# Optimization experiments

Measured on AMD Instinct MI355X. Metric: run time of the kernel, lower is better.

Reference implementation:

```python
import jax, jax.numpy as jnp
import numpy as np

H = 2048          # hidden_size
N = 16384         # batch (= events processed in one forward)
THR = 0.7         # event_threshold
NEG = -1e30       # masked-softmax fill


def setup_inputs() -> dict:
    key = jax.random.key(0)
    ks = jax.random.split(key, 8)
    s = lambda k, shape, scale: (jax.random.normal(k, shape, dtype=jnp.float32) * scale)
    return {
        "x": jax.random.normal(ks[0], (N, H), dtype=jnp.float32),
        "importance": jax.random.uniform(ks[1], (N,), dtype=jnp.float32),
        # event_detector: Linear(H, H//2) -> ReLU -> Linear(H//2, 1) -> Sigmoid
        "W_e1": s(ks[2], (H, H // 2), 0.02), "b_e1": jnp.zeros((H // 2,), jnp.float32),
        "W_e2": s(ks[3], (H // 2, 1), 0.05), "b_e2": jnp.ones((1,), jnp.float32),
        # retrieval_network: Linear(H, H//2) -> ReLU -> Linear(H//2, H) -> Sigmoid
        "W_r1": s(ks[4], (H, H // 2), 0.02), "b_r1": jnp.zeros((H // 2,), jnp.float32),
        "W_r2": s(ks[5], (H // 2, H), 0.02), "b_r2": jnp.zeros((H,), jnp.float32),
        "timestamp": 0,
    }


def reference(x, importance, W_e1, b_e1, W_e2, b_e2, W_r1, b_r1, W_r2, b_r2, timestamp):
    # --- detect_events: MLP -> sigmoid -> threshold -------------------------
    scores = jax.nn.sigmoid(jnp.maximum(x @ W_e1 + b_e1, 0.0) @ W_e2 + b_e2)[:, 0]  # [N]
    events = scores > THR                                   # bool mask = event-gated scatter
    has_events = jnp.any(events)

    # --- store_memory + consolidate_memories --------------------------------
    # Event rows are written into the ring buffer (no wraparound since N <= capacity);
    # consolidation = softmax over stored importances, weighted sum of stored rows.
    logits = jnp.where(events, importance, NEG)             # masked softmax over event rows
    w = jax.nn.softmax(logits)                              # [N]
    w = jnp.where(events, w, 0.0)
    consolidated = w @ x                                    # [H]

    # --- retrieve_memory -----------------------------------------------------
    # After consolidation memory_count == 1, so softmax(similarities) == 1 for
    # every query row and retrieved_memory == consolidated (broadcast to [N,H]).
    retrieved = jax.nn.sigmoid(jnp.maximum(consolidated @ W_r1 + b_r1, 0.0) @ W_r2 + b_r2)  # [H]

    # If no events fired, memory_count == 0 and retrieve_memory returns zeros.
    add = jnp.where(has_events, retrieved, jnp.zeros_like(retrieved))
    return x + add[None, :]
```

## Files before the change

### kernel.cpp

```cpp
#include <hip/hip_runtime.h>
#include <hip/hip_bf16.h>

#define H_    2048
#define NROWS 16384
#define HH    1024

typedef __bf16 bf16x8 __attribute__((ext_vector_type(8)));
typedef float  floatx4 __attribute__((ext_vector_type(4)));

__device__ __forceinline__ unsigned f2bf(float f) {
  unsigned u = __builtin_bit_cast(unsigned, f);
  u += 0x7fff + ((u >> 16) & 1);
  return u >> 16;
}

__device__ __forceinline__ void gload_lds16(const void* g, void* l) {
  __builtin_amdgcn_global_load_lds(
      (const __attribute__((address_space(1))) unsigned*)g,
      (__attribute__((address_space(3))) unsigned*)l, 16, 0, 0);
}

__global__ __launch_bounds__(256) void convert_x_kernel(
    const float* __restrict__ x, unsigned short* __restrict__ xb)
{
  size_t i = ((size_t)blockIdx.x * 256 + threadIdx.x) * 8;
  float4 v0 = *reinterpret_cast<const float4*>(x + i);
  float4 v1 = *reinterpret_cast<const float4*>(x + i + 4);
  uint4 o;
  o.x = f2bf(v0.x) | (f2bf(v0.y) << 16);
  o.y = f2bf(v0.z) | (f2bf(v0.w) << 16);
  o.z = f2bf(v1.x) | (f2bf(v1.y) << 16);
  o.w = f2bf(v1.z) | (f2bf(v1.w) << 16);
  *reinterpret_cast<uint4*>(xb + i) = o;
}

__global__ __launch_bounds__(256) void transpose_w1_kernel(
    const float* __restrict__ W1, unsigned short* __restrict__ W1t)
{
  __shared__ unsigned short tile[64][66];
  int k0 = blockIdx.x * 64;
  int n0 = blockIdx.y * 64;
  int t = threadIdx.x;
#pragma unroll
  for (int i = 0; i < 4; i++) {
    int idx = t + i * 256;
    int r = idx >> 4, c4 = (idx & 15) << 2;
    float4 v = *reinterpret_cast<const float4*>(W1 + (size_t)(k0 + r) * HH + n0 + c4);
    tile[r][c4 + 0] = (unsigned short)f2bf(v.x);
    tile[r][c4 + 1] = (unsigned short)f2bf(v.y);
    tile[r][c4 + 2] = (unsigned short)f2bf(v.z);
    tile[r][c4 + 3] = (unsigned short)f2bf(v.w);
  }
  __syncthreads();
#pragma unroll
  for (int i = 0; i < 2; i++) {
    int idx = t + i * 256;
    int n = idx >> 3, k8 = (idx & 7) << 3;
    uint4 o;
    o.x = (unsigned)tile[k8 + 0][n] | ((unsigned)tile[k8 + 1][n] << 16);
    o.y = (unsigned)tile[k8 + 2][n] | ((unsigned)tile[k8 + 3][n] << 16);
    o.z = (unsigned)tile[k8 + 4][n] | ((unsigned)tile[k8 + 5][n] << 16);
    o.w = (unsigned)tile[k8 + 6][n] | ((unsigned)tile[k8 + 7][n] << 16);
    *reinterpret_cast<uint4*>(W1t + (size_t)(n0 + n) * H_ + k0 + k8) = o;
  }
}

__global__ __launch_bounds__(256) void gemm_v2_kernel(
    const unsigned short* __restrict__ xb, const unsigned short* __restrict__ W1t,
    const float* __restrict__ b1, const float* __restrict__ W2,
    float* __restrict__ s_pre)
{
  __shared__ unsigned short As[128 * 32];
  __shared__ unsigned short Bs[128 * 32];

  const int t    = threadIdx.x;
  const int n0   = blockIdx.x * 128;
  const int m0   = blockIdx.y * 128;
  const int wave = t >> 6, lane = t & 63;
  const int wr   = (wave >> 1) * 64;
  const int wc   = (wave & 1) * 64;
  const int lcol = lane & 15, quad = lane >> 4;

  floatx4 acc[4][4] = {};

  const unsigned short* ag0 = xb  + (size_t)(m0 + (t >> 2)) * H_ + (t & 3) * 8;
  const unsigned short* ag1 = ag0 + (size_t)64 * H_;
  const unsigned short* bg0 = W1t + (size_t)(n0 + (t >> 2)) * H_ + (t & 3) * 8;
  const unsigned short* bg1 = bg0 + (size_t)64 * H_;
  unsigned short* al0 = As + 512 * wave;
  unsigned short* al1 = As + 2048 + 512 * wave;
  unsigned short* bl0 = Bs + 512 * wave;
  unsigned short* bl1 = Bs + 2048 + 512 * wave;

  for (int kk = 0; kk < H_; kk += 32) {
    __syncthreads();
    gload_lds16(ag0 + kk, al0);
    gload_lds16(ag1 + kk, al1);
    gload_lds16(bg0 + kk, bl0);
    gload_lds16(bg1 + kk, bl1);
    __syncthreads();

    bf16x8 af[4], bfr[4];
#pragma unroll
    for (int mt = 0; mt < 4; mt++)
      af[mt] = *reinterpret_cast<const bf16x8*>(As + (wr + mt * 16 + lcol) * 32 + quad * 8);
#pragma unroll
    for (int nt = 0; nt < 4; nt++)
      bfr[nt] = *reinterpret_cast<const bf16x8*>(Bs + (wc + nt * 16 + lcol) * 32 + quad * 8);
#pragma unroll
    for (int mt = 0; mt < 4; mt++)
#pragma unroll
      for (int nt = 0; nt < 4; nt++)
        acc[mt][nt] = __builtin_amdgcn_mfma_f32_16x16x32_bf16(af[mt], bfr[nt], acc[mt][nt], 0, 0, 0);
  }

  float rowsum[4][4];
#pragma unroll
  for (int mt = 0; mt < 4; mt++)
#pragma unroll
    for (int r = 0; r < 4; r++) rowsum[mt][r] = 0.f;

#pragma unroll
  for (int nt = 0; nt < 4; nt++) {
    int n = n0 + wc + nt * 16 + lcol;
    float b1v = b1[n], w2v = W2[n];
#pragma unroll
    for (int mt = 0; mt < 4; mt++)
#pragma unroll
      for (int r = 0; r < 4; r++) {
        float h = fmaxf(acc[mt][nt][r] + b1v, 0.f);
        rowsum[mt][r] = fmaf(h, w2v, rowsum[mt][r]);
      }
  }
#pragma unroll
  for (int mt = 0; mt < 4; mt++)
#pragma unroll
    for (int r = 0; r < 4; r++) {
      float s = rowsum[mt][r];
      s += __shfl_xor(s, 1); s += __shfl_xor(s, 2);
      s += __shfl_xor(s, 4); s += __shfl_xor(s, 8);
      if (lcol == 0)
        atomicAdd(&s_pre[m0 + wr + mt * 16 + quad * 4 + r], s);
    }
}

__global__ __launch_bounds__(256) void gemm_score_kernel(
    const float* __restrict__ x, const float* __restrict__ W1,
    const float* __restrict__ b1, const float* __restrict__ W2,
    float* __restrict__ s_pre)
{
  __shared__ unsigned short As[128][40];
  __shared__ unsigned short Bs[128][40];
  const int t    = threadIdx.x;
  const int n0   = blockIdx.x * 128;
  const int m0   = blockIdx.y * 128;
  const int wave = t >> 6, lane = t & 63;
  const int wr   = (wave >> 1) * 64;
  const int wc   = (wave & 1) * 64;
  const int lcol = lane & 15, quad = lane >> 4;
  floatx4 acc[4][4] = {};

  for (int kk = 0; kk < H_; kk += 32) {
    __syncthreads();
#pragma unroll
    for (int i = 0; i < 4; i++) {
      int idx = t + i * 256;
      int row = idx >> 3, k4 = (idx & 7) << 2;
      float4 v = *reinterpret_cast<const float4*>(x + (size_t)(m0 + row) * H_ + kk + k4);
      unsigned lo = f2bf(v.x) | (f2bf(v.y) << 16);
      unsigned hi = f2bf(v.z) | (f2bf(v.w) << 16);
      *reinterpret_cast<uint2*>(&As[row][k4]) = make_uint2(lo, hi);
    }
#pragma unroll
    for (int i = 0; i < 4; i++) {
      int idx = t + i * 256;
      int kr = idx >> 5, c4 = (idx & 31) << 2;
      float4 v = *reinterpret_cast<const float4*>(W1 + (size_t)(kk + kr) * HH + n0 + c4);
      Bs[c4 + 0][kr] = (unsigned short)f2bf(v.x);
      Bs[c4 + 1][kr] = (unsigned short)f2bf(v.y);
      Bs[c4 + 2][kr] = (unsigned short)f2bf(v.z);
      Bs[c4 + 3][kr] = (unsigned short)f2bf(v.w);
    }
    __syncthreads();
    bf16x8 af[4], bfr[4];
#pragma unroll
    for (int mt = 0; mt < 4; mt++)
      af[mt] = *reinterpret_cast<const bf16x8*>(&As[wr + mt * 16 + lcol][quad * 8]);
#pragma unroll
    for (int nt = 0; nt < 4; nt++)
      bfr[nt] = *reinterpret_cast<const bf16x8*>(&Bs[wc + nt * 16 + lcol][quad * 8]);
#pragma unroll
    for (int mt = 0; mt < 4; mt++)
#pragma unroll
      for (int nt = 0; nt < 4; nt++)
        acc[mt][nt] = __builtin_amdgcn_mfma_f32_16x16x32_bf16(af[mt], bfr[nt], acc[mt][nt], 0, 0, 0);
  }
  float rowsum[4][4];
#pragma unroll
  for (int mt = 0; mt < 4; mt++)
#pragma unroll
    for (int r = 0; r < 4; r++) rowsum[mt][r] = 0.f;
#pragma unroll
  for (int nt = 0; nt < 4; nt++) {
    int n = n0 + wc + nt * 16 + lcol;
    float b1v = b1[n], w2v = W2[n];
#pragma unroll
    for (int mt = 0; mt < 4; mt++)
#pragma unroll
      for (int r = 0; r < 4; r++) {
        float h = fmaxf(acc[mt][nt][r] + b1v, 0.f);
        rowsum[mt][r] = fmaf(h, w2v, rowsum[mt][r]);
      }
  }
#pragma unroll
  for (int mt = 0; mt < 4; mt++)
#pragma unroll
    for (int r = 0; r < 4; r++) {
      float s = rowsum[mt][r];
      s += __shfl_xor(s, 1); s += __shfl_xor(s, 2);
      s += __shfl_xor(s, 4); s += __shfl_xor(s, 8);
      if (lcol == 0)
        atomicAdd(&s_pre[m0 + wr + mt * 16 + quad * 4 + r], s);
    }
}

__global__ __launch_bounds__(256) void score_kernel(
    const float* __restrict__ s_pre, const float* __restrict__ imp,
    const float* __restrict__ b2, float* __restrict__ wbuf,
    float* __restrict__ Z, float* __restrict__ cnt)
{
  int i = blockIdx.x * 256 + threadIdx.x;
  float s = s_pre[i] + b2[0];
  float sig = 1.f / (1.f + __expf(-s));
  bool ev = sig > 0.7f;
  float w = ev ? __expf(imp[i]) : 0.f;
  wbuf[i] = w;
  float cw = ev ? 1.f : 0.f;
#pragma unroll
  for (int off = 32; off; off >>= 1) {
    w  += __shfl_down(w, off);
    cw += __shfl_down(cw, off);
  }
  if ((threadIdx.x & 63) == 0) {
    atomicAdd(Z, w);
    atomicAdd(cnt, cw);
  }
}

__global__ __launch_bounds__(256) void consolidate_kernel(
    const float* __restrict__ x, const float* __restrict__ wbuf,
    float* __restrict__ c)
{
  int t = threadIdx.x;
  int r0 = blockIdx.x * 128;
  float a[8] = {0.f, 0.f, 0.f, 0.f, 0.f, 0.f, 0.f, 0.f};
  for (int r = 0; r < 128; r++) {
    float w = wbuf[r0 + r];
    if (w != 0.f) {
      const float4* xr = reinterpret_cast<const float4*>(x + (size_t)(r0 + r) * H_);
      float4 v0 = xr[t], v1 = xr[t + 256];
      a[0] = fmaf(w, v0.x, a[0]); a[1] = fmaf(w, v0.y, a[1]);
      a[2] = fmaf(w, v0.z, a[2]); a[3] = fmaf(w, v0.w, a[3]);
      a[4] = fmaf(w, v1.x, a[4]); a[5] = fmaf(w, v1.y, a[5]);
      a[6] = fmaf(w, v1.z, a[6]); a[7] = fmaf(w, v1.w, a[7]);
    }
  }
  int j0 = t * 4;
  atomicAdd(&c[j0 + 0], a[0]); atomicAdd(&c[j0 + 1], a[1]);
  atomicAdd(&c[j0 + 2], a[2]); atomicAdd(&c[j0 + 3], a[3]);
  atomicAdd(&c[1024 + j0 + 0], a[4]); atomicAdd(&c[1024 + j0 + 1], a[5]);
  atomicAdd(&c[1024 + j0 + 2], a[6]); atomicAdd(&c[1024 + j0 + 3], a[7]);
}

__global__ __launch_bounds__(256) void r1_kernel(
    const float* __restrict__ c, const float* __restrict__ Z,
    const float* __restrict__ cnt, const float* __restrict__ Wr1,
    float* __restrict__ hr)
{
  __shared__ float cs[128];
  int n  = blockIdx.x * 256 + threadIdx.x;
  int k0 = blockIdx.y * 128;
  float inv = (cnt[0] > 0.5f) ? (1.f / Z[0]) : 0.f;
  if (threadIdx.x < 128) cs[threadIdx.x] = c[k0 + threadIdx.x] * inv;
  __syncthreads();
  float s = 0.f;
#pragma unroll 8
  for (int k = 0; k < 128; k++)
    s = fmaf(cs[k], Wr1[(size_t)(k0 + k) * HH + n], s);
  atomicAdd(&hr[n], s);
}

__global__ __launch_bounds__(256) void r2_kernel(
    const float* __restrict__ hr, const float* __restrict__ br1,
    const float* __restrict__ Wr2, float* __restrict__ rt)
{
  __shared__ float hs[128];
  int n  = blockIdx.x * 256 + threadIdx.x;
  int k0 = blockIdx.y * 128;
  if (threadIdx.x < 128)
    hs[threadIdx.x] = fmaxf(hr[k0 + threadIdx.x] + br1[k0 + threadIdx.x], 0.f);
  __syncthreads();
  float s = 0.f;
#pragma unroll 8
  for (int k = 0; k < 128; k++)
    s = fmaf(hs[k], Wr2[(size_t)(k0 + k) * H_ + n], s);
  atomicAdd(&rt[n], s);
}

__global__ __launch_bounds__(256) void finalize_kernel(
    const float* __restrict__ rt, const float* __restrict__ br2,
    const float* __restrict__ cnt, float* __restrict__ addv)
{
  int j = blockIdx.x * 256 + threadIdx.x;
  float v = 0.f;
  if (cnt[0] > 0.5f) v = 1.f / (1.f + expf(-(rt[j] + br2[j])));
  addv[j] = v;
}

__global__ __launch_bounds__(256) void out_kernel(
    const float* __restrict__ x, const float* __restrict__ addv,
    float* __restrict__ out)
{
  size_t i = (size_t)blockIdx.x * 256 + threadIdx.x;
  int j4 = (int)(i & 511);
  float4 a = reinterpret_cast<const float4*>(addv)[j4];
  float4 v = reinterpret_cast<const float4*>(x)[i];
  v.x += a.x; v.y += a.y; v.z += a.z; v.w += a.w;
  reinterpret_cast<float4*>(out)[i] = v;
}

extern "C" void kernel_launch(void* const* d_in, const int* in_sizes, int n_in,
                              void* d_out, int out_size, void* d_ws, size_t ws_size,
                              hipStream_t stream)
{
  (void)in_sizes; (void)n_in; (void)out_size;
  const float* x   = (const float*)d_in[0];
  const float* imp = (const float*)d_in[1];
  const float* We1 = (const float*)d_in[2];
  const float* be1 = (const float*)d_in[3];
  const float* We2 = (const float*)d_in[4];
  const float* be2 = (const float*)d_in[5];
  const float* Wr1 = (const float*)d_in[6];
  const float* br1 = (const float*)d_in[7];
  const float* Wr2 = (const float*)d_in[8];
  const float* br2 = (const float*)d_in[9];
  float* out = (float*)d_out;

  float* ws    = (float*)d_ws;
  float* s_pre = ws;
  float* c     = ws + 16384;
  float* hr    = ws + 18432;
  float* rt    = ws + 19456;
  float* Z     = ws + 21504;
  float* cnt   = ws + 21505;
  float* wbuf  = ws + 21760;
  float* addv  = ws + 38144;

  const size_t scal_bytes = 49152 * sizeof(float);
  const size_t xb_bytes   = (size_t)NROWS * H_ * 2;
  const size_t w1t_bytes  = (size_t)HH * H_ * 2;
  unsigned short* xb  = (unsigned short*)((char*)d_ws + scal_bytes);
  unsigned short* W1t = (unsigned short*)((char*)d_ws + scal_bytes + xb_bytes);
  const bool fast = ws_size >= scal_bytes + xb_bytes + w1t_bytes;

  hipMemsetAsync(d_ws, 0, 21506 * sizeof(float), stream);

  if (fast) {
    convert_x_kernel<<<16384, 256, 0, stream>>>(x, xb);
    transpose_w1_kernel<<<dim3(32, 16), 256, 0, stream>>>(We1, W1t);
    gemm_v2_kernel<<<dim3(8, 128), 256, 0, stream>>>(xb, W1t, be1, We2, s_pre);
  } else {
    gemm_score_kernel<<<dim3(8, 128), 256, 0, stream>>>(x, We1, be1, We2, s_pre);
  }
  score_kernel<<<64, 256, 0, stream>>>(s_pre, imp, be2, wbuf, Z, cnt);
  consolidate_kernel<<<128, 256, 0, stream>>>(x, wbuf, c);
  r1_kernel<<<dim3(4, 16), 256, 0, stream>>>(c, Z, cnt, Wr1, hr);
  r2_kernel<<<dim3(8, 8), 256, 0, stream>>>(hr, br1, Wr2, rt);
  finalize_kernel<<<8, 256, 0, stream>>>(rt, br2, cnt, addv);
  out_kernel<<<32768, 256, 0, stream>>>(x, addv, out);
}
```

Baseline: 468.7 us.

## Deepen GEMM K-tile to 64 with XOR-swizzled LDS, swap grid order, split consolidate

The bf16 MFMA GEMM now stages a 64-wide K slice per barrier pair instead of 32, halving the number of sync rounds. The LDS layout uses an XOR swizzle on 16-byte chunks to avoid bank conflicts on the fragment reads. The grid is transposed so consecutive blocks share the same W1t column tile, which may change L2 reuse. The consolidate kernel is split into 4x more blocks to add parallelism, at the cost of more atomics on the output vector.

Result: faster. 456.1 us (-2.7%).

```diff
diff --git a/kernel.cpp b/kernel.cpp
--- a/kernel.cpp
+++ b/kernel.cpp
@@ -70,12 +70,12 @@
     const float* __restrict__ b1, const float* __restrict__ W2,
     float* __restrict__ s_pre)
 {
-  __shared__ unsigned short As[128 * 32];
-  __shared__ unsigned short Bs[128 * 32];
+  __shared__ unsigned short As[128 * 64];
+  __shared__ unsigned short Bs[128 * 64];
 
   const int t    = threadIdx.x;
-  const int n0   = blockIdx.x * 128;
-  const int m0   = blockIdx.y * 128;
+  const int m0   = blockIdx.x * 128;
+  const int n0   = blockIdx.y * 128;
   const int wave = t >> 6, lane = t & 63;
   const int wr   = (wave >> 1) * 64;
   const int wc   = (wave & 1) * 64;
@@ -83,35 +83,43 @@
 
   floatx4 acc[4][4] = {};
 
-  const unsigned short* ag0 = xb  + (size_t)(m0 + (t >> 2)) * H_ + (t & 3) * 8;
-  const unsigned short* ag1 = ag0 + (size_t)64 * H_;
-  const unsigned short* bg0 = W1t + (size_t)(n0 + (t >> 2)) * H_ + (t & 3) * 8;
-  const unsigned short* bg1 = bg0 + (size_t)64 * H_;
-  unsigned short* al0 = As + 512 * wave;
-  unsigned short* al1 = As + 2048 + 512 * wave;
-  unsigned short* bl0 = Bs + 512 * wave;
-  unsigned short* bl1 = Bs + 2048 + 512 * wave;
-
-  for (int kk = 0; kk < H_; kk += 32) {
+  const int srow = t >> 3;
+  const int sq   = (t & 7) ^ (srow & 7);
+  const unsigned short* ag = xb  + (size_t)(m0 + srow) * H_ + sq * 8;
+  const unsigned short* bg = W1t + (size_t)(n0 + srow) * H_ + sq * 8;
+  unsigned short* al = As + 512 * wave;
+  unsigned short* bl = Bs + 512 * wave;
+
+  for (int kk = 0; kk < H_; kk += 64) {
     __syncthreads();
-    gload_lds16(ag0 + kk, al0);
-    gload_lds16(ag1 + kk, al1);
-    gload_lds16(bg0 + kk, bl0);
-    gload_lds16(bg1 + kk, bl1);
+#pragma unroll
+    for (int j = 0; j < 4; j++) {
+      gload_lds16(ag + kk + (size_t)(32 * j) * H_, al + 2048 * j);
+      gload_lds16(bg + kk + (size_t)(32 * j) * H_, bl + 2048 * j);
+    }
     __syncthreads();
 
-    bf16x8 af[4], bfr[4];
-#pragma unroll
-    for (int mt = 0; mt < 4; mt++)
-      af[mt] = *reinterpret_cast<const bf16x8*>(As + (wr + mt * 16 + lcol) * 32 + quad * 8);
-#pragma unroll
-    for (int nt = 0; nt < 4; nt++)
-      bfr[nt] = *reinterpret_cast<const bf16x8*>(Bs + (wc + nt * 16 + lcol) * 32 + quad * 8);
-#pragma unroll
-    for (int mt = 0; mt < 4; mt++)
-#pragma unroll
-      for (int nt = 0; nt < 4; nt++)
-        acc[mt][nt] = __builtin_amdgcn_mfma_f32_16x16x32_bf16(af[mt], bfr[nt], acc[mt][nt], 0, 0, 0);
+#pragma unroll
+    for (int h = 0; h < 2; h++) {
+      bf16x8 af[4], bfr[4];
+#pragma unroll
+      for (int mt = 0; mt < 4; mt++) {
+        int r = wr + mt * 16 + lcol;
+        af[mt] = *reinterpret_cast<const bf16x8*>(
+            As + r * 64 + ((((h << 2) | quad) ^ (r & 7)) << 3));
+      }
+#pragma unroll
+      for (int nt = 0; nt < 4; nt++) {
+        int r = wc + nt * 16 + lcol;
+        bfr[nt] = *reinterpret_cast<const bf16x8*>(
+            Bs + r * 64 + ((((h << 2) | quad) ^ (r & 7)) << 3));
+      }
+#pragma unroll
+      for (int mt = 0; mt < 4; mt++)
+#pragma unroll
+        for (int nt = 0; nt < 4; nt++)
+          acc[mt][nt] = __builtin_amdgcn_mfma_f32_16x16x32_bf16(af[mt], bfr[nt], acc[mt][nt], 0, 0, 0);
+    }
   }
 
   float rowsum[4][4];
@@ -252,9 +260,9 @@
     float* __restrict__ c)
 {
   int t = threadIdx.x;
-  int r0 = blockIdx.x * 128;
+  int r0 = blockIdx.x * 32;
   float a[8] = {0.f, 0.f, 0.f, 0.f, 0.f, 0.f, 0.f, 0.f};
-  for (int r = 0; r < 128; r++) {
+  for (int r = 0; r < 32; r++) {
     float w = wbuf[r0 + r];
     if (w != 0.f) {
       const float4* xr = reinterpret_cast<const float4*>(x + (size_t)(r0 + r) * H_);
@@ -368,12 +376,12 @@
   if (fast) {
     convert_x_kernel<<<16384, 256, 0, stream>>>(x, xb);
     transpose_w1_kernel<<<dim3(32, 16), 256, 0, stream>>>(We1, W1t);
-    gemm_v2_kernel<<<dim3(8, 128), 256, 0, stream>>>(xb, W1t, be1, We2, s_pre);
+    gemm_v2_kernel<<<dim3(128, 8), 256, 0, stream>>>(xb, W1t, be1, We2, s_pre);
   } else {
     gemm_score_kernel<<<dim3(8, 128), 256, 0, stream>>>(x, We1, be1, We2, s_pre);
   }
   score_kernel<<<64, 256, 0, stream>>>(s_pre, imp, be2, wbuf, Z, cnt);
-  consolidate_kernel<<<128, 256, 0, stream>>>(x, wbuf, c);
+  consolidate_kernel<<<512, 256, 0, stream>>>(x, wbuf, c);
   r1_kernel<<<dim3(4, 16), 256, 0, stream>>>(c, Z, cnt, Wr1, hr);
   r2_kernel<<<dim3(8, 8), 256, 0, stream>>>(hr, br1, Wr2, rt);
   finalize_kernel<<<8, 256, 0, stream>>>(rt, br2, cnt, addv);
```
